# Kernel optimization log

Measured on AMD Instinct MI355X. Metric: run time of the kernel, lower is better.

## Reference

```python
import jax, jax.numpy as jnp
import numpy as np

NUM_HEADS = 16
WINDOW = 256


def setup_inputs() -> dict:
    key = jax.random.key(0)
    ks = jax.random.split(key, 9)
    B, S, E = 2, 2048, 1024
    sc = 1.0 / np.sqrt(E)
    return {
        "x": jax.random.normal(ks[0], (B, S, E), dtype=jnp.float32),
        "Wq": jax.random.normal(ks[1], (E, E), dtype=jnp.float32) * sc,
        "bq": jnp.zeros((E,), dtype=jnp.float32),
        "Wk": jax.random.normal(ks[2], (E, E), dtype=jnp.float32) * sc,
        "bk": jnp.zeros((E,), dtype=jnp.float32),
        "Wv": jax.random.normal(ks[3], (E, E), dtype=jnp.float32) * sc,
        "bv": jnp.zeros((E,), dtype=jnp.float32),
        "Wo": jax.random.normal(ks[4], (E, E), dtype=jnp.float32) * sc,
        "bo": jnp.zeros((E,), dtype=jnp.float32),
    }


def reference(x, Wq, bq, Wk, bk, Wv, bv, Wo, bo):
    B, S, E = x.shape
    H = NUM_HEADS
    D = E // H
    Q = (x @ Wq + bq).reshape(B, S, H, D).transpose(0, 2, 1, 3)  # [B,H,S,D]
    # Faithful to original: K is view(B, H, S, D), NOT a permute of (B,S,H,D)
    K = (x @ Wk + bk).reshape(B, H, S, D)
    V = (x @ Wv + bv).reshape(B, S, H, D).transpose(0, 2, 1, 3)  # [B,H,S,D]
    scores = jnp.einsum('bhqd,bhkd->bhqk', Q, K) / jnp.sqrt(jnp.float32(D))
    # sliding-window mask: j in [i-W, i+W)  (diag included, i+W exclusive)
    i = jnp.arange(S)[:, None]
    j = jnp.arange(S)[None, :]
    mask = (j >= i - WINDOW) & (j < i + WINDOW)  # [S,S]
    scores = jnp.where(mask, scores, -jnp.inf)
    attn = jax.nn.softmax(scores, axis=-1)
    out = jnp.einsum('bhqk,bhkd->bhqd', attn, V)  # [B,H,S,D]
    out = out.transpose(0, 2, 1, 3).reshape(B, S, E)
    return out @ Wo + bo
```

## Files before the change

kernel.cpp:

```cpp
#include <hip/hip_runtime.h>

#define S_LEN 2048
#define EMB   1024
#define HEADS 16
#define HDIM  64
#define WIN   256

typedef unsigned short u16;
typedef unsigned int   u32;
typedef float  f32x4  __attribute__((ext_vector_type(4)));
typedef __bf16 bf16x8 __attribute__((ext_vector_type(8)));
typedef unsigned short u16x4 __attribute__((ext_vector_type(4)));

typedef const __attribute__((address_space(1))) u32* gas_ptr;
typedef __attribute__((address_space(3))) u32*       las_ptr;

__device__ __forceinline__ void gload16(const void* g, void* l) {
    __builtin_amdgcn_global_load_lds((gas_ptr)g, (las_ptr)l, 16, 0, 0);
}

__device__ __forceinline__ u16 f2bf(float v) {
    u32 x = __builtin_bit_cast(u32, v);
    return (u16)((x + 0x7fffu + ((x >> 16) & 1u)) >> 16);
}
__device__ __forceinline__ u32 cvt_pk_bf16(float lo, float hi) {
    u32 r;
    asm volatile("v_cvt_pk_bf16_f32 %0, %1, %2" : "=v"(r) : "v"(lo), "v"(hi));
    return r;
}

__global__ void convert_bf16_kernel(const float* __restrict__ in,
                                    u16* __restrict__ out, int n4)
{
    int i = blockIdx.x * blockDim.x + threadIdx.x;
    if (i >= n4) return;
    float4 v = reinterpret_cast<const float4*>(in)[i];
    u16x4 o;
    o[0] = f2bf(v.x); o[1] = f2bf(v.y); o[2] = f2bf(v.z); o[3] = f2bf(v.w);
    reinterpret_cast<u16x4*>(out)[i] = o;
}

__global__ __launch_bounds__(256)
void transpose_w_kernel(const float* __restrict__ W0, const float* __restrict__ W1,
                        const float* __restrict__ W2, const float* __restrict__ W3,
                        u16* __restrict__ T0, u16* __restrict__ T1,
                        u16* __restrict__ T2, u16* __restrict__ T3)
{
    const int z = blockIdx.z;
    const float* W = (z == 0) ? W0 : (z == 1) ? W1 : (z == 2) ? W2 : W3;
    u16* T = (z == 0) ? T0 : (z == 1) ? T1 : (z == 2) ? T2 : T3;

    __shared__ float Ts[64][68];
    const int tid = threadIdx.x;
    const int k0 = blockIdx.x * 64, n0 = blockIdx.y * 64;

    int r = tid >> 2, c0 = (tid & 3) * 16;
#pragma unroll
    for (int q = 0; q < 4; ++q) {
        float4 v = *reinterpret_cast<const float4*>(W + (size_t)(k0 + r) * EMB + n0 + c0 + 4 * q);
        *reinterpret_cast<float4*>(&Ts[r][c0 + 4 * q]) = v;
    }
    __syncthreads();

    int n = tid >> 2, kk0 = (tid & 3) * 16;
    u16 hb[16];
#pragma unroll
    for (int e = 0; e < 16; ++e) hb[e] = f2bf(Ts[kk0 + e][n]);
    size_t base = (size_t)(n0 + n) * EMB + k0 + kk0;
#pragma unroll
    for (int q = 0; q < 2; ++q) {
        u32 w[4];
#pragma unroll
        for (int e = 0; e < 4; ++e)
            w[e] = (u32)hb[q * 8 + 2 * e] | ((u32)hb[q * 8 + 2 * e + 1] << 16);
        *reinterpret_cast<uint4*>(T + base + q * 8) = make_uint4(w[0], w[1], w[2], w[3]);
    }
}

template<int NFN, bool OUTBF>
__global__ __launch_bounds__(256, 3)
void mfma_gemm(const u16* __restrict__ A,
               const u16* __restrict__ B0, const u16* __restrict__ B1,
               const u16* __restrict__ B2,
               const float* __restrict__ bias0, const float* __restrict__ bias1,
               const float* __restrict__ bias2,
               float s0, float s1, float s2,
               void* __restrict__ Y0, void* __restrict__ Y1, void* __restrict__ Y2,
               int M, int N, int K)
{
    constexpr int TNB = NFN * 32;

    const int z = blockIdx.z;
    const u16*   Bt   = (z == 0) ? B0 : (z == 1) ? B1 : B2;
    const float* bias = (z == 0) ? bias0 : (z == 1) ? bias1 : bias2;
    const float  scl  = (z == 0) ? s0 : (z == 1) ? s1 : s2;
    void*        Y    = (z == 0) ? Y0 : (z == 1) ? Y1 : Y2;

    __shared__ u16 lds[(128 + TNB) * 32];
    u16* lA = lds;
    u16* lB = lds + 128 * 32;

    const int tid  = threadIdx.x;
    const int wid  = tid >> 6, lane = tid & 63;
    const int wr   = wid >> 1, wc = wid & 1;
    const int lr   = lane & 15, lg = lane >> 4;
    const int bm   = blockIdx.y * 128, bn = blockIdx.x * TNB;

    const int srow = lane >> 2;
    const int scol = (lane & 3) * 8;

    f32x4 acc[4][NFN];
#pragma unroll
    for (int i = 0; i < 4; ++i)
#pragma unroll
        for (int j = 0; j < NFN; ++j) acc[i][j] = (f32x4)0.0f;

    for (int k0 = 0; k0 < K; k0 += 32) {
#pragma unroll
        for (int q = 0; q < 2; ++q) {
            int ch = wid + q * 4;
            gload16(A + (size_t)(bm + ch * 16 + srow) * K + k0 + scol,
                    lA + ch * 512);
        }
#pragma unroll
        for (int q = 0; q < TNB / 64; ++q) {
            int ch = wid + q * 4;
            gload16(Bt + (size_t)(bn + ch * 16 + srow) * K + k0 + scol,
                    lB + ch * 512);
        }
        __syncthreads();

        bf16x8 a0[4], b0[NFN];
#pragma unroll
        for (int mf = 0; mf < 4; ++mf)
            a0[mf] = *reinterpret_cast<const bf16x8*>(
                lA + (wr * 64 + mf * 16 + lr) * 32 + lg * 8);
#pragma unroll
        for (int nf = 0; nf < NFN; ++nf)
            b0[nf] = *reinterpret_cast<const bf16x8*>(
                lB + (wc * NFN * 16 + nf * 16 + lr) * 32 + lg * 8);
#pragma unroll
        for (int mf = 0; mf < 4; ++mf)
#pragma unroll
            for (int nf = 0; nf < NFN; ++nf)
                acc[mf][nf] = __builtin_amdgcn_mfma_f32_16x16x32_bf16(
                    a0[mf], b0[nf], acc[mf][nf], 0, 0, 0);
        __syncthreads();
    }

#pragma unroll
    for (int nf = 0; nf < NFN; ++nf) {
        int col = bn + wc * NFN * 16 + nf * 16 + lr;
        float bs = bias[col];
#pragma unroll
        for (int mf = 0; mf < 4; ++mf) {
#pragma unroll
            for (int r = 0; r < 4; ++r) {
                int row = bm + wr * 64 + mf * 16 + lg * 4 + r;
                float val = (acc[mf][nf][r] + bs) * scl;
                if (OUTBF)
                    ((u16*)Y)[(size_t)row * N + col] = f2bf(val);
                else
                    ((float*)Y)[(size_t)row * N + col] = val;
            }
        }
    }
}

__global__ __launch_bounds__(256, 4)
void attn_mfma_kernel(const u16* __restrict__ Qb, const u16* __restrict__ Kb,
                      const u16* __restrict__ Vb, u16* __restrict__ AOh)
{
    __shared__ u16 Ks[64 * 64];
    __shared__ u16 Vt[64 * 64];
    __shared__ u16 Ps[4 * 16 * 64];

    constexpr float L2E = 1.44269504f;

    const int nwg = gridDim.x * gridDim.y * gridDim.z;
    int n  = blockIdx.x + gridDim.x * (blockIdx.y + gridDim.y * blockIdx.z);
    int sw = (n & 7) * (nwg >> 3) + (n >> 3);
    const int qb = sw & 31;
    const int h  = (sw >> 5) & 15;
    const int b  = sw >> 9;

    const int i0  = qb * 64;
    const int tid = threadIdx.x;
    const int wid = tid >> 6, lane = tid & 63;
    const int lr  = lane & 15, lg = lane >> 4;
    const int l7  = lr & 7;

    const u16* Kh = Kb + (size_t)b * S_LEN * EMB + (size_t)h * S_LEN * HDIM;

    bf16x8 qa[2];
    {
        const u16* qp = Qb + ((size_t)(b * S_LEN + i0 + wid * 16 + lr)) * EMB
                        + h * HDIM + lg * 8;
        qa[0] = *reinterpret_cast<const bf16x8*>(qp);
        qa[1] = *reinterpret_cast<const bf16x8*>(qp + 32);
    }

    float m2 = -1e30f, l = 0.0f;
    f32x4 o[4];
#pragma unroll
    for (int nf = 0; nf < 4; ++nf) o[nf] = (f32x4)0.0f;

    const int tlo = (qb < 4) ? 0 : qb - 4;
    const int thi = (qb > 27) ? 31 : qb + 4;
    const int qg  = i0 + wid * 16 + lr;

    for (int t = tlo; t <= thi; ++t) {
        __syncthreads();

#pragma unroll
        for (int q = 0; q < 2; ++q) {
            int cc = tid + q * 256;
            int j = cc >> 3, g = cc & 7;
            uint4 v = *reinterpret_cast<const uint4*>(
                Kh + (size_t)(t * 64 + j) * HDIM + g * 8);
            *reinterpret_cast<uint4*>(Ks + j * 64 + ((g ^ (j & 7)) << 3)) = v;
        }
        {
            int jp = (tid & 31) * 2, dc = tid >> 5;
            const u16* vp = Vb + ((size_t)(b * S_LEN + t * 64 + jp)) * EMB
                            + h * HDIM + dc * 8;
            uint4 r0 = *reinterpret_cast<const uint4*>(vp);
            uint4 r1 = *reinterpret_cast<const uint4*>(vp + EMB);
            const u16* e0 = reinterpret_cast<const u16*>(&r0);
            const u16* e1 = reinterpret_cast<const u16*>(&r1);
            int jg = jp >> 3, jl = jp & 7;
#pragma unroll
            for (int e = 0; e < 8; ++e) {
                int d = dc * 8 + e;
                u32 w = (u32)e0[e] | ((u32)e1[e] << 16);
                *reinterpret_cast<u32*>(Vt + d * 64 + ((jg ^ (d & 7)) << 3) + jl) = w;
            }
        }
        __syncthreads();

        f32x4 s[4];
#pragma unroll
        for (int nf = 0; nf < 4; ++nf) s[nf] = (f32x4)0.0f;
#pragma unroll
        for (int ks = 0; ks < 2; ++ks) {
            int cg = (ks * 4 + lg) ^ l7;
#pragma unroll
            for (int nf = 0; nf < 4; ++nf) {
                bf16x8 kf = *reinterpret_cast<const bf16x8*>(
                    Ks + (nf * 16 + lr) * 64 + (cg << 3));
                s[nf] = __builtin_amdgcn_mfma_f32_16x16x32_bf16(kf, qa[ks], s[nf], 0, 0, 0);
            }
        }

        if (t == qb - 4 || t == qb + 4) {
            int klo = qg - WIN, khi = qg + WIN;
#pragma unroll
            for (int nf = 0; nf < 4; ++nf) {
#pragma unroll
                for (int r = 0; r < 4; ++r) {
                    int kg = t * 64 + nf * 16 + lg * 4 + r;
                    bool ok = (kg >= klo) && (kg < khi);
                    s[nf][r] = ok ? s[nf][r] : -1e30f;
                }
            }
        }

        float tmax = s[0][0];
#pragma unroll
        for (int nf = 0; nf < 4; ++nf)
#pragma unroll
            for (int r = 0; r < 4; ++r) tmax = fmaxf(tmax, s[nf][r]);
        tmax = fmaxf(tmax, __shfl_xor(tmax, 16));
        tmax = fmaxf(tmax, __shfl_xor(tmax, 32));
        float tmax2 = tmax * L2E;

        bool need = tmax2 > m2 + 12.0f;
        if (__any(need)) {
            float mn2 = fmaxf(m2, tmax2);
            float sc = __builtin_amdgcn_exp2f(m2 - mn2);
            m2 = mn2;
            l *= sc;
#pragma unroll
            for (int r = 0; r < 4; ++r) {
                float scr = __shfl(sc, lg * 4 + r);
#pragma unroll
                for (int nf = 0; nf < 4; ++nf) o[nf][r] *= scr;
            }
        }

        float ps = 0.0f;
#pragma unroll
        for (int nf = 0; nf < 4; ++nf) {
            float p0 = __builtin_amdgcn_exp2f(fmaf(s[nf][0], L2E, -m2));
            float p1 = __builtin_amdgcn_exp2f(fmaf(s[nf][1], L2E, -m2));
            float p2 = __builtin_amdgcn_exp2f(fmaf(s[nf][2], L2E, -m2));
            float p3 = __builtin_amdgcn_exp2f(fmaf(s[nf][3], L2E, -m2));
            ps += (p0 + p1) + (p2 + p3);
            u32 pk0 = cvt_pk_bf16(p0, p1);
            u32 pk1 = cvt_pk_bf16(p2, p3);
            int idx16 = wid * 1024 + lr * 64 +
                        (((nf * 2 + (lg >> 1)) ^ l7) << 3) + (lg & 1) * 4;
            *reinterpret_cast<uint2*>(Ps + idx16) = make_uint2(pk0, pk1);
        }
        ps += __shfl_xor(ps, 16);
        ps += __shfl_xor(ps, 32);
        l += ps;

#pragma unroll
        for (int ks = 0; ks < 2; ++ks) {
            int cg = (ks * 4 + lg) ^ l7;
            bf16x8 pf = *reinterpret_cast<const bf16x8*>(
                Ps + wid * 1024 + lr * 64 + (cg << 3));
#pragma unroll
            for (int nf = 0; nf < 4; ++nf) {
                bf16x8 vf = *reinterpret_cast<const bf16x8*>(
                    Vt + (nf * 16 + lr) * 64 + (cg << 3));
                o[nf] = __builtin_amdgcn_mfma_f32_16x16x32_bf16(pf, vf, o[nf], 0, 0, 0);
            }
        }
    }

    float inv = 1.0f / l;
#pragma unroll
    for (int r = 0; r < 4; ++r) {
        float invr = __shfl(inv, lg * 4 + r);
#pragma unroll
        for (int nf = 0; nf < 4; ++nf) {
            size_t idx = ((size_t)(b * S_LEN + i0 + wid * 16 + lg * 4 + r)) * EMB
                         + h * HDIM + nf * 16 + lr;
            AOh[idx] = f2bf(o[nf][r] * invr);
        }
    }
}

extern "C" void kernel_launch(void* const* d_in, const int* in_sizes, int n_in,
                              void* d_out, int out_size, void* d_ws, size_t ws_size,
                              hipStream_t stream)
{
    (void)n_in; (void)out_size; (void)ws_size;
    const float* x  = (const float*)d_in[0];
    const float* Wq = (const float*)d_in[1];
    const float* bq = (const float*)d_in[2];
    const float* Wk = (const float*)d_in[3];
    const float* bk = (const float*)d_in[4];
    const float* Wv = (const float*)d_in[5];
    const float* bv = (const float*)d_in[6];
    const float* Wo = (const float*)d_in[7];
    const float* bo = (const float*)d_in[8];
    float* out = (float*)d_out;

    const int B = in_sizes[0] / (S_LEN * EMB);
    const int M = B * S_LEN;

    u16* xh  = (u16*)d_ws;
    u16* WtQ = xh  + (size_t)M * EMB;
    u16* WtK = WtQ + (size_t)EMB * EMB;
    u16* WtV = WtK + (size_t)EMB * EMB;
    u16* WtO = WtV + (size_t)EMB * EMB;
    u16* Qb  = WtO + (size_t)EMB * EMB;
    u16* Kb  = Qb + (size_t)M * EMB;
    u16* Vb  = Kb + (size_t)M * EMB;
    u16* AOh = Vb + (size_t)M * EMB;

    int n4 = M * EMB / 4;
    convert_bf16_kernel<<<n4 / 256, 256, 0, stream>>>(x, xh, n4);

    dim3 gt(EMB / 64, EMB / 64, 4);
    transpose_w_kernel<<<gt, 256, 0, stream>>>(Wq, Wk, Wv, Wo, WtQ, WtK, WtV, WtO);

    dim3 g1(EMB / 128, M / 128, 3);
    mfma_gemm<4, true><<<g1, 256, 0, stream>>>(
        xh, WtQ, WtK, WtV, bq, bk, bv, 0.125f, 1.0f, 1.0f,
        Qb, Kb, Vb, M, EMB, EMB);

    dim3 g2(S_LEN / 64, HEADS, B);
    attn_mfma_kernel<<<g2, 256, 0, stream>>>(Qb, Kb, Vb, AOh);

    dim3 g3(EMB / 64, M / 128, 1);
    mfma_gemm<2, false><<<g3, 256, 0, stream>>>(
        AOh, WtO, WtO, WtO, bo, bo, bo, 1.0f, 1.0f, 1.0f,
        out, out, out, M, EMB, EMB);
}
```

Measured before the change: 92.20 us.

## Enlarge attention query tile to 128 rows and fuse input prep kernels

The attention kernel now handles 128 query rows per block with 512 threads (8 waves). Each 64-key K/V tile loaded into shared memory is reused across twice as many queries, and the K tile is loaded with direct global-to-LDS transfers. The x bf16 conversion is merged into the weight transpose kernel as an extra z-slice, saving a launch. Costs: the key range covers 10 tiles instead of 9 per 128 queries, so some tiles are mostly masked and mask checks run on more tiles. The grid is also halved, which reduces parallelism.

```diff
diff --git a/kernel.cpp b/kernel.cpp
--- a/kernel.cpp
+++ b/kernel.cpp
@@ -29,29 +29,31 @@
     return r;
 }
 
-__global__ void convert_bf16_kernel(const float* __restrict__ in,
-                                    u16* __restrict__ out, int n4)
-{
-    int i = blockIdx.x * blockDim.x + threadIdx.x;
-    if (i >= n4) return;
-    float4 v = reinterpret_cast<const float4*>(in)[i];
-    u16x4 o;
-    o[0] = f2bf(v.x); o[1] = f2bf(v.y); o[2] = f2bf(v.z); o[3] = f2bf(v.w);
-    reinterpret_cast<u16x4*>(out)[i] = o;
-}
-
 __global__ __launch_bounds__(256)
-void transpose_w_kernel(const float* __restrict__ W0, const float* __restrict__ W1,
-                        const float* __restrict__ W2, const float* __restrict__ W3,
-                        u16* __restrict__ T0, u16* __restrict__ T1,
-                        u16* __restrict__ T2, u16* __restrict__ T3)
+void prep_kernel(const float* __restrict__ W0, const float* __restrict__ W1,
+                 const float* __restrict__ W2, const float* __restrict__ W3,
+                 u16* __restrict__ T0, u16* __restrict__ T1,
+                 u16* __restrict__ T2, u16* __restrict__ T3,
+                 const float* __restrict__ x, u16* __restrict__ xh, int n4)
 {
     const int z = blockIdx.z;
+    const int tid = threadIdx.x;
+
+    if (z == 4) {
+        int bid = blockIdx.x + 16 * blockIdx.y;
+        for (int i = bid * 256 + tid; i < n4; i += 65536) {
+            float4 v = reinterpret_cast<const float4*>(x)[i];
+            u16x4 o;
+            o[0] = f2bf(v.x); o[1] = f2bf(v.y); o[2] = f2bf(v.z); o[3] = f2bf(v.w);
+            reinterpret_cast<u16x4*>(xh)[i] = o;
+        }
+        return;
+    }
+
     const float* W = (z == 0) ? W0 : (z == 1) ? W1 : (z == 2) ? W2 : W3;
     u16* T = (z == 0) ? T0 : (z == 1) ? T1 : (z == 2) ? T2 : T3;
 
     __shared__ float Ts[64][68];
-    const int tid = threadIdx.x;
     const int k0 = blockIdx.x * 64, n0 = blockIdx.y * 64;
 
     int r = tid >> 2, c0 = (tid & 3) * 16;
@@ -167,24 +169,24 @@
     }
 }
 
-__global__ __launch_bounds__(256, 4)
+__global__ __launch_bounds__(512, 4)
 void attn_mfma_kernel(const u16* __restrict__ Qb, const u16* __restrict__ Kb,
                       const u16* __restrict__ Vb, u16* __restrict__ AOh)
 {
     __shared__ u16 Ks[64 * 64];
     __shared__ u16 Vt[64 * 64];
-    __shared__ u16 Ps[4 * 16 * 64];
+    __shared__ u16 Ps[8 * 16 * 64];
 
     constexpr float L2E = 1.44269504f;
 
     const int nwg = gridDim.x * gridDim.y * gridDim.z;
     int n  = blockIdx.x + gridDim.x * (blockIdx.y + gridDim.y * blockIdx.z);
     int sw = (n & 7) * (nwg >> 3) + (n >> 3);
-    const int qb = sw & 31;
-    const int h  = (sw >> 5) & 15;
-    const int b  = sw >> 9;
-
-    const int i0  = qb * 64;
+    const int qb = sw & 15;
+    const int h  = (sw >> 4) & 15;
+    const int b  = sw >> 8;
+
+    const int i0  = qb * 128;
     const int tid = threadIdx.x;
     const int wid = tid >> 6, lane = tid & 63;
     const int lr  = lane & 15, lg = lane >> 4;
@@ -205,33 +207,31 @@
 #pragma unroll
     for (int nf = 0; nf < 4; ++nf) o[nf] = (f32x4)0.0f;
 
-    const int tlo = (qb < 4) ? 0 : qb - 4;
-    const int thi = (qb > 27) ? 31 : qb + 4;
+    const int tlo = (2 * qb < 4) ? 0 : 2 * qb - 4;
+    const int thi = (2 * qb + 5 > 31) ? 31 : 2 * qb + 5;
     const int qg  = i0 + wid * 16 + lr;
+
+    const int kj   = lane >> 3;
+    const int kgsw = (lane & 7) ^ kj;
 
     for (int t = tlo; t <= thi; ++t) {
         __syncthreads();
 
-#pragma unroll
-        for (int q = 0; q < 2; ++q) {
-            int cc = tid + q * 256;
-            int j = cc >> 3, g = cc & 7;
-            uint4 v = *reinterpret_cast<const uint4*>(
-                Kh + (size_t)(t * 64 + j) * HDIM + g * 8);
-            *reinterpret_cast<uint4*>(Ks + j * 64 + ((g ^ (j & 7)) << 3)) = v;
-        }
+        gload16(Kh + (size_t)(t * 64 + wid * 8 + kj) * HDIM + kgsw * 8,
+                Ks + wid * 512);
+
         {
             int jp = (tid & 31) * 2, dc = tid >> 5;
             const u16* vp = Vb + ((size_t)(b * S_LEN + t * 64 + jp)) * EMB
-                            + h * HDIM + dc * 8;
-            uint4 r0 = *reinterpret_cast<const uint4*>(vp);
-            uint4 r1 = *reinterpret_cast<const uint4*>(vp + EMB);
+                            + h * HDIM + dc * 4;
+            uint2 r0 = *reinterpret_cast<const uint2*>(vp);
+            uint2 r1 = *reinterpret_cast<const uint2*>(vp + EMB);
             const u16* e0 = reinterpret_cast<const u16*>(&r0);
             const u16* e1 = reinterpret_cast<const u16*>(&r1);
             int jg = jp >> 3, jl = jp & 7;
 #pragma unroll
-            for (int e = 0; e < 8; ++e) {
-                int d = dc * 8 + e;
+            for (int e = 0; e < 4; ++e) {
+                int d = dc * 4 + e;
                 u32 w = (u32)e0[e] | ((u32)e1[e] << 16);
                 *reinterpret_cast<u32*>(Vt + d * 64 + ((jg ^ (d & 7)) << 3) + jl) = w;
             }
@@ -252,7 +252,7 @@
             }
         }
 
-        if (t == qb - 4 || t == qb + 4) {
+        if (t <= 2 * qb - 3 || t >= 2 * qb + 4) {
             int klo = qg - WIN, khi = qg + WIN;
 #pragma unroll
             for (int nf = 0; nf < 4; ++nf) {
@@ -363,18 +363,17 @@
     u16* AOh = Vb + (size_t)M * EMB;
 
     int n4 = M * EMB / 4;
-    convert_bf16_kernel<<<n4 / 256, 256, 0, stream>>>(x, xh, n4);
-
-    dim3 gt(EMB / 64, EMB / 64, 4);
-    transpose_w_kernel<<<gt, 256, 0, stream>>>(Wq, Wk, Wv, Wo, WtQ, WtK, WtV, WtO);
+    dim3 gt(EMB / 64, EMB / 64, 5);
+    prep_kernel<<<gt, 256, 0, stream>>>(Wq, Wk, Wv, Wo, WtQ, WtK, WtV, WtO,
+                                        x, xh, n4);
 
     dim3 g1(EMB / 128, M / 128, 3);
     mfma_gemm<4, true><<<g1, 256, 0, stream>>>(
         xh, WtQ, WtK, WtV, bq, bk, bv, 0.125f, 1.0f, 1.0f,
         Qb, Kb, Vb, M, EMB, EMB);
 
-    dim3 g2(S_LEN / 64, HEADS, B);
-    attn_mfma_kernel<<<g2, 256, 0, stream>>>(Qb, Kb, Vb, AOh);
+    dim3 g2(S_LEN / 128, HEADS, B);
+    attn_mfma_kernel<<<g2, 512, 0, stream>>>(Qb, Kb, Vb, AOh);
 
     dim3 g3(EMB / 64, M / 128, 1);
     mfma_gemm<2, false><<<g3, 256, 0, stream>>>(
```

Result: no change. 93.49 us (+1.4%).
